# Kernel optimization log

Measured on AMD Instinct MI355X. Metric: run time of the kernel, lower is better.

## Reference

```python
import jax, jax.numpy as jnp
import numpy as np

DIM, HEADS, FEAT = 512, 8, 128
HEAD_DIM = DIM // HEADS
B, N = 1, 2048
EPS = 1e-8


def setup_inputs() -> dict:
    key = jax.random.key(0)
    k1, k2, k3, k4 = jax.random.split(key, 4)
    x = jax.random.normal(k1, (B, N, DIM), dtype=jnp.float32)
    proj_matrix = jax.random.normal(k2, (HEADS, HEAD_DIM, FEAT), dtype=jnp.float32) / np.sqrt(HEAD_DIM)
    W_qkv = jax.random.normal(k3, (DIM, 3 * DIM), dtype=jnp.float32) * np.sqrt(2.0 / DIM)
    W_out = jax.random.normal(k4, (DIM, DIM), dtype=jnp.float32) * np.sqrt(2.0 / DIM)
    b_out = jnp.zeros((DIM,), dtype=jnp.float32)
    return {"x": x, "proj_matrix": proj_matrix, "W_qkv": W_qkv, "W_out": W_out, "b_out": b_out}


def _feature_map(t):
    return jax.nn.elu(t) + 1.0


def reference(x, proj_matrix, W_qkv, W_out, b_out):
    b, n, d = x.shape
    h, hd = HEADS, HEAD_DIM
    qkv = x @ W_qkv                      # (b,n,3d)
    q, k, v = jnp.split(qkv, 3, axis=-1)
    # (b,n,d) -> (b,h,n,hd)
    def to_heads(t):
        return t.reshape(b, n, h, hd).transpose(0, 2, 1, 3)
    q, k, v = to_heads(q), to_heads(k), to_heads(v)
    q_proj = _feature_map(jnp.einsum('bhnd,hdf->bhnf', q, proj_matrix))
    k_proj = _feature_map(jnp.einsum('bhnd,hdf->bhnf', k, proj_matrix))
    # causal linear attention via prefix sums (matches torch cumsum branch)
    k_cum = jnp.cumsum(k_proj, axis=2)                                   # (b,h,n,f)
    kv_cum = jnp.cumsum(k_proj[..., None] * v[..., None, :], axis=2)     # (b,h,n,f,hd)
    attn = jnp.einsum('bhnf,bhnfd->bhnd', q_proj, kv_cum)
    denom = jnp.einsum('bhnf,bhnf->bhn', q_proj, k_cum)[..., None]
    attn = attn / (denom + EPS)
    attn = attn.transpose(0, 2, 1, 3).reshape(b, n, d)
    return attn @ W_out + b_out
```

## Files before the change

kernel.cpp:

```cpp
#include <hip/hip_runtime.h>
#include <math.h>

#define NTOK 2048
#define DMODEL 512
#define NH 8
#define HD 64
#define NF 128
#define QKV_LD 1536
#define CHUNK 64
#define NCHUNK 32
#define EPS_C 1e-8f

typedef __bf16 bf16x8 __attribute__((ext_vector_type(8)));
typedef float f32x4 __attribute__((ext_vector_type(4)));

__device__ inline unsigned short f2bf(float f) {
  union { float f; unsigned u; } v; v.f = f;
  unsigned r = v.u + 0x7FFF + ((v.u >> 16) & 1);
  return (unsigned short)(r >> 16);
}


__global__ __launch_bounds__(256) void pack_all(
    const float* __restrict__ x, const float* __restrict__ W_qkv,
    const float* __restrict__ W_out, const float* __restrict__ proj,
    unsigned short* __restrict__ xpk, unsigned short* __restrict__ wqkvpk,
    unsigned short* __restrict__ woutpk, unsigned short* __restrict__ projpk,
    unsigned short* __restrict__ vT_pk)
{
  const int tid = blockIdx.x * 256 + threadIdx.x;
  const int job = blockIdx.y;
  unsigned short o[8];
  if (job == 0) {
    if (tid >= 131072) return;
    const int lane = tid & 63, blk = tid >> 6;
    const int bk = blk & 15, bm = blk >> 4;
    const int m = bm * 16 + (lane & 15), k = bk * 32 + (lane >> 4) * 8;
    const float4 v0 = *(const float4*)&x[(size_t)m * 512 + k];
    const float4 v1 = *(const float4*)&x[(size_t)m * 512 + k + 4];
    o[0] = f2bf(v0.x); o[1] = f2bf(v0.y); o[2] = f2bf(v0.z); o[3] = f2bf(v0.w);
    o[4] = f2bf(v1.x); o[5] = f2bf(v1.y); o[6] = f2bf(v1.z); o[7] = f2bf(v1.w);
    *(ushort4*)&xpk[(size_t)tid * 8]     = *(ushort4*)&o[0];
    *(ushort4*)&xpk[(size_t)tid * 8 + 4] = *(ushort4*)&o[4];
  } else if (job == 1) {
    if (tid >= 98304) return;
    const int lane = tid & 63, blk = tid >> 6;
    const int bk = blk & 15, bn = blk >> 4;
    const int n = bn * 16 + (lane & 15), k = bk * 32 + (lane >> 4) * 8;
#pragma unroll
    for (int e = 0; e < 8; ++e) o[e] = f2bf(W_qkv[(size_t)(k + e) * QKV_LD + n]);
    *(ushort4*)&wqkvpk[(size_t)tid * 8]     = *(ushort4*)&o[0];
    *(ushort4*)&wqkvpk[(size_t)tid * 8 + 4] = *(ushort4*)&o[4];
  } else if (job == 2) {
    if (tid >= 32768) return;
    const int lane = tid & 63, blk = tid >> 6;
    const int bk = blk & 15, bn = blk >> 4;
    const int n = bn * 16 + (lane & 15), k = bk * 32 + (lane >> 4) * 8;
#pragma unroll
    for (int e = 0; e < 8; ++e) o[e] = f2bf(W_out[(size_t)(k + e) * DMODEL + n]);
    *(ushort4*)&woutpk[(size_t)tid * 8]     = *(ushort4*)&o[0];
    *(ushort4*)&woutpk[(size_t)tid * 8 + 4] = *(ushort4*)&o[4];
  } else if (job == 3) {
    if (tid >= 8192) return;
    const int lane = tid & 63, blk = (tid >> 6) & 15, h = tid >> 10;
    const int bk = blk & 1, bn = blk >> 1;
    const int n = bn * 16 + (lane & 15), k = bk * 32 + (lane >> 4) * 8;
#pragma unroll
    for (int e = 0; e < 8; ++e) o[e] = f2bf(proj[(size_t)h * HD * NF + (size_t)(k + e) * NF + n]);
    *(ushort4*)&projpk[(size_t)tid * 8]     = *(ushort4*)&o[0];
    *(ushort4*)&projpk[(size_t)tid * 8 + 4] = *(ushort4*)&o[4];
  } else {
    if (tid >= 32768) return;
    const int hc = tid >> 7, kt = (tid >> 6) & 1, lane = tid & 63;
    const unsigned short val = ((lane & 15) == 0) ? (unsigned short)0x3F80 : (unsigned short)0;
    const size_t u = (size_t)hc * 640 + (4 * 2 + kt) * 64 + lane;
#pragma unroll
    for (int e = 0; e < 8; ++e) o[e] = val;
    *(ushort4*)&vT_pk[u * 8]     = *(ushort4*)&o[0];
    *(ushort4*)&vT_pk[u * 8 + 4] = *(ushort4*)&o[4];
  }
}

__global__ __launch_bounds__(256) void qkv_proj(
    const unsigned short* __restrict__ Apk, const unsigned short* __restrict__ Bpk,
    const unsigned short* __restrict__ projpk,
    unsigned short* __restrict__ q_pk, unsigned short* __restrict__ k_pk,
    unsigned short* __restrict__ kT_pk, unsigned short* __restrict__ vT_pk)
{
  __shared__ unsigned short QK[4096];
  const int lane = threadIdx.x & 63, w = threadIdx.x >> 6;
  const int wr = w >> 1, wc = w & 1;
  const int c = blockIdx.y;
  const int m0 = c * 64 + wr * 32;
  const int n0 = blockIdx.x * 64 + wc * 32;
  const unsigned short* a0 = Apk + ((size_t)(m0 >> 4) * 16 * 64 + lane) * 8;
  const unsigned short* a1 = a0 + (size_t)16 * 512;
  const unsigned short* b0 = Bpk + ((size_t)(n0 >> 4) * 16 * 64 + lane) * 8;
  const unsigned short* b1 = b0 + (size_t)16 * 512;
  f32x4 acc00 = {0.f, 0.f, 0.f, 0.f}, acc01 = acc00, acc10 = acc00, acc11 = acc00;
#pragma unroll 4
  for (int s = 0; s < 16; ++s) {
    const bf16x8 af0 = *(const bf16x8*)(a0 + (size_t)s * 512);
    const bf16x8 af1 = *(const bf16x8*)(a1 + (size_t)s * 512);
    const bf16x8 bv0 = *(const bf16x8*)(b0 + (size_t)s * 512);
    const bf16x8 bv1 = *(const bf16x8*)(b1 + (size_t)s * 512);
    acc00 = __builtin_amdgcn_mfma_f32_16x16x32_bf16(af0, bv0, acc00, 0, 0, 0);
    acc01 = __builtin_amdgcn_mfma_f32_16x16x32_bf16(af0, bv1, acc01, 0, 0, 0);
    acc10 = __builtin_amdgcn_mfma_f32_16x16x32_bf16(af1, bv0, acc10, 0, 0, 0);
    acc11 = __builtin_amdgcn_mfma_f32_16x16x32_bf16(af1, bv1, acc11, 0, 0, 0);
  }
  const int r16 = lane & 15, kg = lane >> 4;
  if (blockIdx.x < 16) {
    const int src = blockIdx.x >> 3, h = blockIdx.x & 7;
#pragma unroll
    for (int mb = 0; mb < 2; ++mb) {
#pragma unroll
      for (int nb = 0; nb < 2; ++nb) {
        const f32x4 a = mb == 0 ? (nb == 0 ? acc00 : acc01) : (nb == 0 ? acc10 : acc11);
        const size_t u = ((size_t)(wr * 2 + mb) * 2 + wc) * 64 +
                         (nb * 2 + (r16 >> 3)) * 16 + kg * 4;
        const int elem = r16 & 7;
#pragma unroll
        for (int r = 0; r < 4; ++r)
          QK[(u + r) * 8 + elem] = f2bf(a[r]);
      }
    }
    __syncthreads();
    const unsigned short* bbase = projpk + (size_t)h * 8192 + (size_t)lane * 8;
    f32x4 p[2][4] = {};
#pragma unroll
    for (int s = 0; s < 2; ++s) {
#pragma unroll
      for (int mb = 0; mb < 2; ++mb) {
        const bf16x8 af = *(const bf16x8*)&QK[((((size_t)(wr * 2 + mb)) * 2 + s) * 64 + lane) * 8];
#pragma unroll
        for (int nb = 0; nb < 4; ++nb) {
          const bf16x8 bv = *(const bf16x8*)(bbase + (size_t)((wc * 4 + nb) * 2 + s) * 512);
          p[mb][nb] = __builtin_amdgcn_mfma_f32_16x16x32_bf16(af, bv, p[mb][nb], 0, 0, 0);
        }
      }
    }
    unsigned short* dst = (src ? k_pk : q_pk) + (size_t)h * 262144;
#pragma unroll
    for (int mb = 0; mb < 2; ++mb) {
#pragma unroll
      for (int nb = 0; nb < 4; ++nb) {
        unsigned short vb[4];
#pragma unroll
        for (int r = 0; r < 4; ++r) {
          const float v = p[mb][nb][r];
          vb[r] = f2bf(v > 0.f ? v + 1.f : expf(v));
        }
        const size_t base = ((size_t)(c * 4 + wr * 2 + mb) * 4 + wc * 2 + (nb >> 1)) * 64 +
                            ((nb & 1) * 2 + (r16 >> 3)) * 16;
        const int elem = r16 & 7;
#pragma unroll
        for (int r = 0; r < 4; ++r)
          dst[(base + kg * 4 + r) * 8 + elem] = vb[r];
        if (src == 1) {
          const size_t u = (size_t)(h * 32 + c) * 1024 +
              ((size_t)(wc * 4 + nb) * 2 + wr) * 64 + r16 + (mb * 2 + (kg >> 1)) * 16;
          *(ushort4*)&kT_pk[u * 8 + (kg & 1) * 4] = *(ushort4*)&vb[0];
        }
      }
    }
  } else {
    const int h = blockIdx.x - 16;
#pragma unroll
    for (int mb = 0; mb < 2; ++mb) {
#pragma unroll
      for (int nb = 0; nb < 2; ++nb) {
        const f32x4 a = mb == 0 ? (nb == 0 ? acc00 : acc01) : (nb == 0 ? acc10 : acc11);
        const int vc = wc * 32 + nb * 16 + r16;
        const size_t u = (size_t)(h * 32 + c) * 640 +
            ((size_t)(vc >> 4) * 2 + wr) * 64 + (vc & 15) + (mb * 2 + (kg >> 1)) * 16;
        ushort4 rr;
        rr.x = f2bf(a[0]); rr.y = f2bf(a[1]); rr.z = f2bf(a[2]); rr.w = f2bf(a[3]);
        *(ushort4*)&vT_pk[u * 8 + (kg & 1) * 4] = rr;
      }
    }
  }
}

__global__ __launch_bounds__(256) void sums_scan(
    const unsigned short* __restrict__ kT_pk, const unsigned short* __restrict__ vT_pk,
    unsigned short* __restrict__ kvpre_pk)
{
  const int lane = threadIdx.x & 63, w = threadIdx.x >> 6;
  const int vt = blockIdx.x, h = blockIdx.y;
  const int r16 = lane & 15, kg = lane >> 4;
  f32x4 acc[2] = {};
  for (int c = 0; c < NCHUNK; ++c) {
    unsigned short* dst = kvpre_pk + (size_t)(h * 32 + c) * 1280 * 8;
#pragma unroll
    for (int mb = 0; mb < 2; ++mb) {
      unsigned short vb[4];
#pragma unroll
      for (int r = 0; r < 4; ++r) vb[r] = f2bf(acc[mb][r]);
      const size_t u = (size_t)(vt * 4 + w) * 64 + r16 + (mb * 2 + (kg >> 1)) * 16;
      *(ushort4*)&dst[u * 8 + (kg & 1) * 4] = *(ushort4*)&vb[0];
    }
    const unsigned short* kb = kT_pk + (size_t)(h * 32 + c) * 1024 * 8;
    const unsigned short* vb_ = vT_pk + (size_t)(h * 32 + c) * 640 * 8;
#pragma unroll
    for (int s = 0; s < 2; ++s) {
      const bf16x8 bf = *(const bf16x8*)(vb_ + (((size_t)vt * 2 + s) * 64 + lane) * 8);
#pragma unroll
      for (int mb = 0; mb < 2; ++mb) {
        const bf16x8 af = *(const bf16x8*)(kb + ((((size_t)(w * 2 + mb)) * 2 + s) * 64 + lane) * 8);
        acc[mb] = __builtin_amdgcn_mfma_f32_16x16x32_bf16(af, bf, acc[mb], 0, 0, 0);
      }
    }
  }
}

__global__ __launch_bounds__(256) void gemm_out(
    const unsigned short* __restrict__ Apk, const unsigned short* __restrict__ Bpk,
    const float* __restrict__ bias, float* __restrict__ Cf, int K, int ldc)
{
  const int lane = threadIdx.x & 63, w = threadIdx.x >> 6;
  const int wr = w >> 1, wc = w & 1;
  const int m0 = blockIdx.y * 64 + wr * 32;
  const int n0 = blockIdx.x * 64 + wc * 32;
  const int ks = K >> 5;
  const unsigned short* a0 = Apk + ((size_t)(m0 >> 4) * ks * 64 + lane) * 8;
  const unsigned short* a1 = a0 + (size_t)ks * 512;
  const unsigned short* b0 = Bpk + ((size_t)(n0 >> 4) * ks * 64 + lane) * 8;
  const unsigned short* b1 = b0 + (size_t)ks * 512;
  f32x4 acc00 = {0.f, 0.f, 0.f, 0.f}, acc01 = acc00, acc10 = acc00, acc11 = acc00;
#pragma unroll 4
  for (int s = 0; s < ks; ++s) {
    const bf16x8 af0 = *(const bf16x8*)(a0 + (size_t)s * 512);
    const bf16x8 af1 = *(const bf16x8*)(a1 + (size_t)s * 512);
    const bf16x8 bv0 = *(const bf16x8*)(b0 + (size_t)s * 512);
    const bf16x8 bv1 = *(const bf16x8*)(b1 + (size_t)s * 512);
    acc00 = __builtin_amdgcn_mfma_f32_16x16x32_bf16(af0, bv0, acc00, 0, 0, 0);
    acc01 = __builtin_amdgcn_mfma_f32_16x16x32_bf16(af0, bv1, acc01, 0, 0, 0);
    acc10 = __builtin_amdgcn_mfma_f32_16x16x32_bf16(af1, bv0, acc10, 0, 0, 0);
    acc11 = __builtin_amdgcn_mfma_f32_16x16x32_bf16(af1, bv1, acc11, 0, 0, 0);
  }
  const int r16 = lane & 15, kg = lane >> 4;
#pragma unroll
  for (int mb = 0; mb < 2; ++mb) {
#pragma unroll
    for (int nb = 0; nb < 2; ++nb) {
      const f32x4 a = mb == 0 ? (nb == 0 ? acc00 : acc01) : (nb == 0 ? acc10 : acc11);
      const int col = n0 + nb * 16 + r16;
      const float bv = bias[col];
#pragma unroll
      for (int r = 0; r < 4; ++r)
        Cf[(size_t)(m0 + mb * 16 + kg * 4 + r) * ldc + col] = a[r] + bv;
    }
  }
}

__global__ __launch_bounds__(256) void chunk_attn(
    const unsigned short* __restrict__ q_pk, const unsigned short* __restrict__ k_pk,
    const unsigned short* __restrict__ kvpre_pk, const unsigned short* __restrict__ vT_pk,
    unsigned short* __restrict__ attn_pk)
{
  __shared__ unsigned short P[4096];
  __shared__ float den[64];
  const int lane = threadIdx.x & 63, w = threadIdx.x >> 6;
  const int wr = w >> 1, wc = w & 1;
  const int c = blockIdx.x, h = blockIdx.y;
  const int r16 = lane & 15, kg = lane >> 4;
  const unsigned short* qb = q_pk + (size_t)h * 262144;
  const unsigned short* kb = k_pk + (size_t)h * 262144;
  bf16x8 qa[2][4];
#pragma unroll
  for (int amb = 0; amb < 2; ++amb)
#pragma unroll
    for (int ks = 0; ks < 4; ++ks)
      qa[amb][ks] = *(const bf16x8*)(qb +
          (((size_t)(c * 4 + wr * 2 + amb) * 4 + ks) * 64 + lane) * 8);
  {
    f32x4 accS[2][2] = {};
#pragma unroll
    for (int ks = 0; ks < 4; ++ks) {
#pragma unroll
      for (int bnb = 0; bnb < 2; ++bnb) {
        const bf16x8 bf = *(const bf16x8*)(kb +
            (((size_t)(c * 4 + wc * 2 + bnb) * 4 + ks) * 64 + lane) * 8);
#pragma unroll
        for (int amb = 0; amb < 2; ++amb)
          accS[amb][bnb] = __builtin_amdgcn_mfma_f32_16x16x32_bf16(qa[amb][ks], bf, accS[amb][bnb], 0, 0, 0);
      }
    }
#pragma unroll
    for (int amb = 0; amb < 2; ++amb)
#pragma unroll
      for (int bnb = 0; bnb < 2; ++bnb) {
        const int ck = wc * 32 + bnb * 16 + r16;
        const size_t u = ((size_t)(wr * 2 + amb) * 2 + wc) * 64 + (bnb * 2 + (r16 >> 3)) * 16;
        const int elem = r16 & 7;
#pragma unroll
        for (int r = 0; r < 4; ++r) {
          const int rq = wr * 32 + amb * 16 + kg * 4 + r;
          P[(u + kg * 4 + r) * 8 + elem] = (ck <= rq) ? f2bf(accS[amb][bnb][r]) : (unsigned short)0;
        }
      }
  }
  __syncthreads();
  const int nnt = wc ? 2 : 3;
  const int ntb = wc ? 3 : 0;
  const unsigned short* kvp = kvpre_pk + (size_t)(h * 32 + c) * 1280 * 8;
  const unsigned short* vtb = vT_pk + (size_t)(h * 32 + c) * 640 * 8;
  f32x4 acc[2][3] = {};
#pragma unroll
  for (int ks = 0; ks < 4; ++ks) {
    bf16x8 bfr[3];
    for (int j = 0; j < 3; ++j)
      if (j < nnt)
        bfr[j] = *(const bf16x8*)(kvp + (((size_t)(ntb + j) * 4 + ks) * 64 + lane) * 8);
#pragma unroll
    for (int amb = 0; amb < 2; ++amb)
      for (int j = 0; j < 3; ++j)
        if (j < nnt)
          acc[amb][j] = __builtin_amdgcn_mfma_f32_16x16x32_bf16(qa[amb][ks], bfr[j], acc[amb][j], 0, 0, 0);
  }
#pragma unroll
  for (int ks = 0; ks < 2; ++ks) {
    bf16x8 bfr[3];
    for (int j = 0; j < 3; ++j)
      if (j < nnt)
        bfr[j] = *(const bf16x8*)(vtb + (((size_t)(ntb + j) * 2 + ks) * 64 + lane) * 8);
#pragma unroll
    for (int amb = 0; amb < 2; ++amb) {
      const bf16x8 pf = *(const bf16x8*)&P[((((size_t)(wr * 2 + amb)) * 2 + ks) * 64 + lane) * 8];
      for (int j = 0; j < 3; ++j)
        if (j < nnt)
          acc[amb][j] = __builtin_amdgcn_mfma_f32_16x16x32_bf16(pf, bfr[j], acc[amb][j], 0, 0, 0);
    }
  }
  if (wc == 1 && r16 == 0) {
#pragma unroll
    for (int amb = 0; amb < 2; ++amb)
#pragma unroll
      for (int r = 0; r < 4; ++r)
        den[wr * 32 + amb * 16 + kg * 4 + r] = acc[amb][1][r] + EPS_C;
  }
  __syncthreads();
#pragma unroll
  for (int amb = 0; amb < 2; ++amb) {
    for (int j = 0; j < 3; ++j) {
      const int nt = ntb + j;
      if (nt >= 4 || j >= nnt) continue;
      const int acol = h * 64 + nt * 16 + r16;
      const size_t base = ((size_t)(c * 4 + wr * 2 + amb) * 16 + (acol >> 5)) * 64 +
                          ((nt * 2 + (r16 >> 3)) & 3) * 16;
      const int elem = acol & 7;
#pragma unroll
      for (int r = 0; r < 4; ++r) {
        const float dinv = 1.0f / den[wr * 32 + amb * 16 + kg * 4 + r];
        attn_pk[(base + kg * 4 + r) * 8 + elem] = f2bf(acc[amb][j][r] * dinv);
      }
    }
  }
}

extern "C" void kernel_launch(void* const* d_in, const int* in_sizes, int n_in,
                              void* d_out, int out_size, void* d_ws, size_t ws_size,
                              hipStream_t stream) {
  const float* x     = (const float*)d_in[0];
  const float* proj  = (const float*)d_in[1];
  const float* W_qkv = (const float*)d_in[2];
  const float* W_out = (const float*)d_in[3];
  const float* b_out = (const float*)d_in[4];
  float* out = (float*)d_out;

  unsigned short* xpk      = (unsigned short*)d_ws;
  unsigned short* wqkvpk   = xpk + 1048576;
  unsigned short* woutpk   = wqkvpk + 786432;
  unsigned short* projpk   = woutpk + 262144;
  unsigned short* q_pk     = projpk + 65536;
  unsigned short* k_pk     = q_pk + 2097152;
  unsigned short* kT_pk    = k_pk + 2097152;
  unsigned short* vT_pk    = kT_pk + 2097152;
  unsigned short* kvpre_pk = vT_pk + 1310720;
  unsigned short* attn_pk  = kvpre_pk + 2621440;

  pack_all<<<dim3(512, 5), 256, 0, stream>>>(x, W_qkv, W_out, proj,
                                             xpk, wqkvpk, woutpk, projpk, vT_pk);
  qkv_proj<<<dim3(QKV_LD / 64, NTOK / 64), 256, 0, stream>>>(
      xpk, wqkvpk, projpk, q_pk, k_pk, kT_pk, vT_pk);
  sums_scan<<<dim3(5, NH), 256, 0, stream>>>(kT_pk, vT_pk, kvpre_pk);
  chunk_attn<<<dim3(NCHUNK, NH), 256, 0, stream>>>(
      q_pk, k_pk, kvpre_pk, vT_pk, attn_pk);
  gemm_out<<<dim3(DMODEL / 64, NTOK / 64), 256, 0, stream>>>(
      attn_pk, woutpk, b_out, out, DMODEL, DMODEL);
}
```

Measured before the change: 52.56 us.

## Fuse all five stages into one cooperative persistent kernel with grid syncs

Turns the five separate kernels into device functions with grid-stride loops and runs them inside one cooperative kernel, separated by grid-wide barriers. The grid is sized from occupancy queries (256 CUs times up to 3 blocks each). If the cooperative launch fails, it falls back to separate launches. The goal is to remove the launch gaps between stages, at the cost of grid-sync overhead, a persistent grid that may be too large for tiny phases like the 40-block scan, and an occupancy query on every call.

```diff
diff --git a/kernel.cpp b/kernel.cpp
--- a/kernel.cpp
+++ b/kernel.cpp
@@ -1,5 +1,8 @@
 #include <hip/hip_runtime.h>
+#include <hip/hip_cooperative_groups.h>
 #include <math.h>
+
+namespace cg = cooperative_groups;
 
 #define NTOK 2048
 #define DMODEL 512
@@ -21,343 +24,398 @@
 }
 
 
-__global__ __launch_bounds__(256) void pack_all(
-    const float* __restrict__ x, const float* __restrict__ W_qkv,
-    const float* __restrict__ W_out, const float* __restrict__ proj,
-    unsigned short* __restrict__ xpk, unsigned short* __restrict__ wqkvpk,
-    unsigned short* __restrict__ woutpk, unsigned short* __restrict__ projpk,
-    unsigned short* __restrict__ vT_pk)
-{
-  const int tid = blockIdx.x * 256 + threadIdx.x;
-  const int job = blockIdx.y;
-  unsigned short o[8];
-  if (job == 0) {
-    if (tid >= 131072) return;
-    const int lane = tid & 63, blk = tid >> 6;
-    const int bk = blk & 15, bm = blk >> 4;
-    const int m = bm * 16 + (lane & 15), k = bk * 32 + (lane >> 4) * 8;
-    const float4 v0 = *(const float4*)&x[(size_t)m * 512 + k];
-    const float4 v1 = *(const float4*)&x[(size_t)m * 512 + k + 4];
-    o[0] = f2bf(v0.x); o[1] = f2bf(v0.y); o[2] = f2bf(v0.z); o[3] = f2bf(v0.w);
-    o[4] = f2bf(v1.x); o[5] = f2bf(v1.y); o[6] = f2bf(v1.z); o[7] = f2bf(v1.w);
-    *(ushort4*)&xpk[(size_t)tid * 8]     = *(ushort4*)&o[0];
-    *(ushort4*)&xpk[(size_t)tid * 8 + 4] = *(ushort4*)&o[4];
-  } else if (job == 1) {
-    if (tid >= 98304) return;
-    const int lane = tid & 63, blk = tid >> 6;
-    const int bk = blk & 15, bn = blk >> 4;
-    const int n = bn * 16 + (lane & 15), k = bk * 32 + (lane >> 4) * 8;
-#pragma unroll
-    for (int e = 0; e < 8; ++e) o[e] = f2bf(W_qkv[(size_t)(k + e) * QKV_LD + n]);
-    *(ushort4*)&wqkvpk[(size_t)tid * 8]     = *(ushort4*)&o[0];
-    *(ushort4*)&wqkvpk[(size_t)tid * 8 + 4] = *(ushort4*)&o[4];
-  } else if (job == 2) {
-    if (tid >= 32768) return;
-    const int lane = tid & 63, blk = tid >> 6;
-    const int bk = blk & 15, bn = blk >> 4;
-    const int n = bn * 16 + (lane & 15), k = bk * 32 + (lane >> 4) * 8;
-#pragma unroll
-    for (int e = 0; e < 8; ++e) o[e] = f2bf(W_out[(size_t)(k + e) * DMODEL + n]);
-    *(ushort4*)&woutpk[(size_t)tid * 8]     = *(ushort4*)&o[0];
-    *(ushort4*)&woutpk[(size_t)tid * 8 + 4] = *(ushort4*)&o[4];
-  } else if (job == 3) {
-    if (tid >= 8192) return;
-    const int lane = tid & 63, blk = (tid >> 6) & 15, h = tid >> 10;
-    const int bk = blk & 1, bn = blk >> 1;
-    const int n = bn * 16 + (lane & 15), k = bk * 32 + (lane >> 4) * 8;
-#pragma unroll
-    for (int e = 0; e < 8; ++e) o[e] = f2bf(proj[(size_t)h * HD * NF + (size_t)(k + e) * NF + n]);
-    *(ushort4*)&projpk[(size_t)tid * 8]     = *(ushort4*)&o[0];
-    *(ushort4*)&projpk[(size_t)tid * 8 + 4] = *(ushort4*)&o[4];
-  } else {
-    if (tid >= 32768) return;
-    const int hc = tid >> 7, kt = (tid >> 6) & 1, lane = tid & 63;
-    const unsigned short val = ((lane & 15) == 0) ? (unsigned short)0x3F80 : (unsigned short)0;
-    const size_t u = (size_t)hc * 640 + (4 * 2 + kt) * 64 + lane;
-#pragma unroll
-    for (int e = 0; e < 8; ++e) o[e] = val;
-    *(ushort4*)&vT_pk[u * 8]     = *(ushort4*)&o[0];
-    *(ushort4*)&vT_pk[u * 8 + 4] = *(ushort4*)&o[4];
-  }
-}
-
-__global__ __launch_bounds__(256) void qkv_proj(
-    const unsigned short* __restrict__ Apk, const unsigned short* __restrict__ Bpk,
-    const unsigned short* __restrict__ projpk,
-    unsigned short* __restrict__ q_pk, unsigned short* __restrict__ k_pk,
-    unsigned short* __restrict__ kT_pk, unsigned short* __restrict__ vT_pk)
+__device__ void ph_pack(
+    const float* x, const float* W_qkv, const float* W_out, const float* proj,
+    unsigned short* xpk, unsigned short* wqkvpk, unsigned short* woutpk,
+    unsigned short* projpk, unsigned short* vT_pk)
+{
+  for (int v = blockIdx.x; v < 1184; v += gridDim.x) {
+    unsigned short o[8];
+    if (v < 512) {
+      const int tid = v * 256 + threadIdx.x;
+      const int lane = tid & 63, blk = tid >> 6;
+      const int bk = blk & 15, bm = blk >> 4;
+      const int m = bm * 16 + (lane & 15), k = bk * 32 + (lane >> 4) * 8;
+      const float4 v0 = *(const float4*)&x[(size_t)m * 512 + k];
+      const float4 v1 = *(const float4*)&x[(size_t)m * 512 + k + 4];
+      o[0] = f2bf(v0.x); o[1] = f2bf(v0.y); o[2] = f2bf(v0.z); o[3] = f2bf(v0.w);
+      o[4] = f2bf(v1.x); o[5] = f2bf(v1.y); o[6] = f2bf(v1.z); o[7] = f2bf(v1.w);
+      *(ushort4*)&xpk[(size_t)tid * 8]     = *(ushort4*)&o[0];
+      *(ushort4*)&xpk[(size_t)tid * 8 + 4] = *(ushort4*)&o[4];
+    } else if (v < 896) {
+      const int tid = (v - 512) * 256 + threadIdx.x;
+      const int lane = tid & 63, blk = tid >> 6;
+      const int bk = blk & 15, bn = blk >> 4;
+      const int n = bn * 16 + (lane & 15), k = bk * 32 + (lane >> 4) * 8;
+#pragma unroll
+      for (int e = 0; e < 8; ++e) o[e] = f2bf(W_qkv[(size_t)(k + e) * QKV_LD + n]);
+      *(ushort4*)&wqkvpk[(size_t)tid * 8]     = *(ushort4*)&o[0];
+      *(ushort4*)&wqkvpk[(size_t)tid * 8 + 4] = *(ushort4*)&o[4];
+    } else if (v < 1024) {
+      const int tid = (v - 896) * 256 + threadIdx.x;
+      const int lane = tid & 63, blk = tid >> 6;
+      const int bk = blk & 15, bn = blk >> 4;
+      const int n = bn * 16 + (lane & 15), k = bk * 32 + (lane >> 4) * 8;
+#pragma unroll
+      for (int e = 0; e < 8; ++e) o[e] = f2bf(W_out[(size_t)(k + e) * DMODEL + n]);
+      *(ushort4*)&woutpk[(size_t)tid * 8]     = *(ushort4*)&o[0];
+      *(ushort4*)&woutpk[(size_t)tid * 8 + 4] = *(ushort4*)&o[4];
+    } else if (v < 1056) {
+      const int tid = (v - 1024) * 256 + threadIdx.x;
+      const int lane = tid & 63, blk = (tid >> 6) & 15, h = tid >> 10;
+      const int bk = blk & 1, bn = blk >> 1;
+      const int n = bn * 16 + (lane & 15), k = bk * 32 + (lane >> 4) * 8;
+#pragma unroll
+      for (int e = 0; e < 8; ++e) o[e] = f2bf(proj[(size_t)h * HD * NF + (size_t)(k + e) * NF + n]);
+      *(ushort4*)&projpk[(size_t)tid * 8]     = *(ushort4*)&o[0];
+      *(ushort4*)&projpk[(size_t)tid * 8 + 4] = *(ushort4*)&o[4];
+    } else {
+      const int tid = (v - 1056) * 256 + threadIdx.x;
+      const int hc = tid >> 7, kt = (tid >> 6) & 1, lane = tid & 63;
+      const unsigned short val = ((lane & 15) == 0) ? (unsigned short)0x3F80 : (unsigned short)0;
+      const size_t u = (size_t)hc * 640 + (4 * 2 + kt) * 64 + lane;
+#pragma unroll
+      for (int e = 0; e < 8; ++e) o[e] = val;
+      *(ushort4*)&vT_pk[u * 8]     = *(ushort4*)&o[0];
+      *(ushort4*)&vT_pk[u * 8 + 4] = *(ushort4*)&o[4];
+    }
+  }
+}
+
+__device__ void ph_qkvproj(
+    const unsigned short* Apk, const unsigned short* Bpk,
+    const unsigned short* projpk, unsigned short* q_pk, unsigned short* k_pk,
+    unsigned short* kT_pk, unsigned short* vT_pk)
 {
   __shared__ unsigned short QK[4096];
   const int lane = threadIdx.x & 63, w = threadIdx.x >> 6;
   const int wr = w >> 1, wc = w & 1;
-  const int c = blockIdx.y;
-  const int m0 = c * 64 + wr * 32;
-  const int n0 = blockIdx.x * 64 + wc * 32;
-  const unsigned short* a0 = Apk + ((size_t)(m0 >> 4) * 16 * 64 + lane) * 8;
-  const unsigned short* a1 = a0 + (size_t)16 * 512;
-  const unsigned short* b0 = Bpk + ((size_t)(n0 >> 4) * 16 * 64 + lane) * 8;
-  const unsigned short* b1 = b0 + (size_t)16 * 512;
-  f32x4 acc00 = {0.f, 0.f, 0.f, 0.f}, acc01 = acc00, acc10 = acc00, acc11 = acc00;
+  const int r16 = lane & 15, kg = lane >> 4;
+  for (int j = blockIdx.x; j < 768; j += gridDim.x) {
+    const int bx = j % 24, c = j / 24;
+    const int m0 = c * 64 + wr * 32;
+    const int n0 = bx * 64 + wc * 32;
+    const unsigned short* a0 = Apk + ((size_t)(m0 >> 4) * 16 * 64 + lane) * 8;
+    const unsigned short* a1 = a0 + (size_t)16 * 512;
+    const unsigned short* b0 = Bpk + ((size_t)(n0 >> 4) * 16 * 64 + lane) * 8;
+    const unsigned short* b1 = b0 + (size_t)16 * 512;
+    f32x4 acc00 = {0.f, 0.f, 0.f, 0.f}, acc01 = acc00, acc10 = acc00, acc11 = acc00;
 #pragma unroll 4
-  for (int s = 0; s < 16; ++s) {
-    const bf16x8 af0 = *(const bf16x8*)(a0 + (size_t)s * 512);
-    const bf16x8 af1 = *(const bf16x8*)(a1 + (size_t)s * 512);
-    const bf16x8 bv0 = *(const bf16x8*)(b0 + (size_t)s * 512);
-    const bf16x8 bv1 = *(const bf16x8*)(b1 + (size_t)s * 512);
-    acc00 = __builtin_amdgcn_mfma_f32_16x16x32_bf16(af0, bv0, acc00, 0, 0, 0);
-    acc01 = __builtin_amdgcn_mfma_f32_16x16x32_bf16(af0, bv1, acc01, 0, 0, 0);
-    acc10 = __builtin_amdgcn_mfma_f32_16x16x32_bf16(af1, bv0, acc10, 0, 0, 0);
-    acc11 = __builtin_amdgcn_mfma_f32_16x16x32_bf16(af1, bv1, acc11, 0, 0, 0);
-  }
+    for (int s = 0; s < 16; ++s) {
+      const bf16x8 af0 = *(const bf16x8*)(a0 + (size_t)s * 512);
+      const bf16x8 af1 = *(const bf16x8*)(a1 + (size_t)s * 512);
+      const bf16x8 bv0 = *(const bf16x8*)(b0 + (size_t)s * 512);
+      const bf16x8 bv1 = *(const bf16x8*)(b1 + (size_t)s * 512);
+      acc00 = __builtin_amdgcn_mfma_f32_16x16x32_bf16(af0, bv0, acc00, 0, 0, 0);
+      acc01 = __builtin_amdgcn_mfma_f32_16x16x32_bf16(af0, bv1, acc01, 0, 0, 0);
+      acc10 = __builtin_amdgcn_mfma_f32_16x16x32_bf16(af1, bv0, acc10, 0, 0, 0);
+      acc11 = __builtin_amdgcn_mfma_f32_16x16x32_bf16(af1, bv1, acc11, 0, 0, 0);
+    }
+    if (bx < 16) {
+      const int src = bx >> 3, h = bx & 7;
+#pragma unroll
+      for (int mb = 0; mb < 2; ++mb) {
+#pragma unroll
+        for (int nb = 0; nb < 2; ++nb) {
+          const f32x4 a = mb == 0 ? (nb == 0 ? acc00 : acc01) : (nb == 0 ? acc10 : acc11);
+          const size_t u = ((size_t)(wr * 2 + mb) * 2 + wc) * 64 +
+                           (nb * 2 + (r16 >> 3)) * 16 + kg * 4;
+          const int elem = r16 & 7;
+#pragma unroll
+          for (int r = 0; r < 4; ++r)
+            QK[(u + r) * 8 + elem] = f2bf(a[r]);
+        }
+      }
+      __syncthreads();
+      const unsigned short* bbase = projpk + (size_t)h * 8192 + (size_t)lane * 8;
+      f32x4 p[2][4] = {};
+#pragma unroll
+      for (int s = 0; s < 2; ++s) {
+#pragma unroll
+        for (int mb = 0; mb < 2; ++mb) {
+          const bf16x8 af = *(const bf16x8*)&QK[((((size_t)(wr * 2 + mb)) * 2 + s) * 64 + lane) * 8];
+#pragma unroll
+          for (int nb = 0; nb < 4; ++nb) {
+            const bf16x8 bv = *(const bf16x8*)(bbase + (size_t)((wc * 4 + nb) * 2 + s) * 512);
+            p[mb][nb] = __builtin_amdgcn_mfma_f32_16x16x32_bf16(af, bv, p[mb][nb], 0, 0, 0);
+          }
+        }
+      }
+      unsigned short* dst = (src ? k_pk : q_pk) + (size_t)h * 262144;
+#pragma unroll
+      for (int mb = 0; mb < 2; ++mb) {
+#pragma unroll
+        for (int nb = 0; nb < 4; ++nb) {
+          unsigned short vb[4];
+#pragma unroll
+          for (int r = 0; r < 4; ++r) {
+            const float vv = p[mb][nb][r];
+            vb[r] = f2bf(vv > 0.f ? vv + 1.f : expf(vv));
+          }
+          const size_t base = ((size_t)(c * 4 + wr * 2 + mb) * 4 + wc * 2 + (nb >> 1)) * 64 +
+                              ((nb & 1) * 2 + (r16 >> 3)) * 16;
+          const int elem = r16 & 7;
+#pragma unroll
+          for (int r = 0; r < 4; ++r)
+            dst[(base + kg * 4 + r) * 8 + elem] = vb[r];
+          if (src == 1) {
+            const size_t u = (size_t)(h * 32 + c) * 1024 +
+                ((size_t)(wc * 4 + nb) * 2 + wr) * 64 + r16 + (mb * 2 + (kg >> 1)) * 16;
+            *(ushort4*)&kT_pk[u * 8 + (kg & 1) * 4] = *(ushort4*)&vb[0];
+          }
+        }
+      }
+      __syncthreads();
+    } else {
+      const int h = bx - 16;
+#pragma unroll
+      for (int mb = 0; mb < 2; ++mb) {
+#pragma unroll
+        for (int nb = 0; nb < 2; ++nb) {
+          const f32x4 a = mb == 0 ? (nb == 0 ? acc00 : acc01) : (nb == 0 ? acc10 : acc11);
+          const int vc = wc * 32 + nb * 16 + r16;
+          const size_t u = (size_t)(h * 32 + c) * 640 +
+              ((size_t)(vc >> 4) * 2 + wr) * 64 + (vc & 15) + (mb * 2 + (kg >> 1)) * 16;
+          ushort4 rr;
+          rr.x = f2bf(a[0]); rr.y = f2bf(a[1]); rr.z = f2bf(a[2]); rr.w = f2bf(a[3]);
+          *(ushort4*)&vT_pk[u * 8 + (kg & 1) * 4] = rr;
+        }
+      }
+    }
+  }
+}
+
+__device__ void ph_scan(
+    const unsigned short* kT_pk, const unsigned short* vT_pk,
+    unsigned short* kvpre_pk)
+{
+  const int lane = threadIdx.x & 63, w = threadIdx.x >> 6;
   const int r16 = lane & 15, kg = lane >> 4;
-  if (blockIdx.x < 16) {
-    const int src = blockIdx.x >> 3, h = blockIdx.x & 7;
-#pragma unroll
-    for (int mb = 0; mb < 2; ++mb) {
-#pragma unroll
-      for (int nb = 0; nb < 2; ++nb) {
-        const f32x4 a = mb == 0 ? (nb == 0 ? acc00 : acc01) : (nb == 0 ? acc10 : acc11);
-        const size_t u = ((size_t)(wr * 2 + mb) * 2 + wc) * 64 +
-                         (nb * 2 + (r16 >> 3)) * 16 + kg * 4;
-        const int elem = r16 & 7;
-#pragma unroll
-        for (int r = 0; r < 4; ++r)
-          QK[(u + r) * 8 + elem] = f2bf(a[r]);
-      }
-    }
-    __syncthreads();
-    const unsigned short* bbase = projpk + (size_t)h * 8192 + (size_t)lane * 8;
-    f32x4 p[2][4] = {};
-#pragma unroll
-    for (int s = 0; s < 2; ++s) {
+  for (int j = blockIdx.x; j < 40; j += gridDim.x) {
+    const int vt = j % 5, h = j / 5;
+    f32x4 acc[2] = {};
+    for (int c = 0; c < NCHUNK; ++c) {
+      unsigned short* dst = kvpre_pk + (size_t)(h * 32 + c) * 1280 * 8;
 #pragma unroll
       for (int mb = 0; mb < 2; ++mb) {
-        const bf16x8 af = *(const bf16x8*)&QK[((((size_t)(wr * 2 + mb)) * 2 + s) * 64 + lane) * 8];
-#pragma unroll
-        for (int nb = 0; nb < 4; ++nb) {
-          const bf16x8 bv = *(const bf16x8*)(bbase + (size_t)((wc * 4 + nb) * 2 + s) * 512);
-          p[mb][nb] = __builtin_amdgcn_mfma_f32_16x16x32_bf16(af, bv, p[mb][nb], 0, 0, 0);
-        }
-      }
-    }
-    unsigned short* dst = (src ? k_pk : q_pk) + (size_t)h * 262144;
-#pragma unroll
-    for (int mb = 0; mb < 2; ++mb) {
-#pragma unroll
-      for (int nb = 0; nb < 4; ++nb) {
         unsigned short vb[4];
 #pragma unroll
-        for (int r = 0; r < 4; ++r) {
-          const float v = p[mb][nb][r];
-          vb[r] = f2bf(v > 0.f ? v + 1.f : expf(v));
-        }
-        const size_t base = ((size_t)(c * 4 + wr * 2 + mb) * 4 + wc * 2 + (nb >> 1)) * 64 +
-                            ((nb & 1) * 2 + (r16 >> 3)) * 16;
-        const int elem = r16 & 7;
-#pragma unroll
-        for (int r = 0; r < 4; ++r)
-          dst[(base + kg * 4 + r) * 8 + elem] = vb[r];
-        if (src == 1) {
-          const size_t u = (size_t)(h * 32 + c) * 1024 +
-              ((size_t)(wc * 4 + nb) * 2 + wr) * 64 + r16 + (mb * 2 + (kg >> 1)) * 16;
-          *(ushort4*)&kT_pk[u * 8 + (kg & 1) * 4] = *(ushort4*)&vb[0];
-        }
-      }
-    }
-  } else {
-    const int h = blockIdx.x - 16;
-#pragma unroll
-    for (int mb = 0; mb < 2; ++mb) {
-#pragma unroll
-      for (int nb = 0; nb < 2; ++nb) {
-        const f32x4 a = mb == 0 ? (nb == 0 ? acc00 : acc01) : (nb == 0 ? acc10 : acc11);
-        const int vc = wc * 32 + nb * 16 + r16;
-        const size_t u = (size_t)(h * 32 + c) * 640 +
-            ((size_t)(vc >> 4) * 2 + wr) * 64 + (vc & 15) + (mb * 2 + (kg >> 1)) * 16;
-        ushort4 rr;
-        rr.x = f2bf(a[0]); rr.y = f2bf(a[1]); rr.z = f2bf(a[2]); rr.w = f2bf(a[3]);
-        *(ushort4*)&vT_pk[u * 8 + (kg & 1) * 4] = rr;
-      }
-    }
-  }
-}
-
-__global__ __launch_bounds__(256) void sums_scan(
-    const unsigned short* __restrict__ kT_pk, const unsigned short* __restrict__ vT_pk,
-    unsigned short* __restrict__ kvpre_pk)
-{
-  const int lane = threadIdx.x & 63, w = threadIdx.x >> 6;
-  const int vt = blockIdx.x, h = blockIdx.y;
-  const int r16 = lane & 15, kg = lane >> 4;
-  f32x4 acc[2] = {};
-  for (int c = 0; c < NCHUNK; ++c) {
-    unsigned short* dst = kvpre_pk + (size_t)(h * 32 + c) * 1280 * 8;
-#pragma unroll
-    for (int mb = 0; mb < 2; ++mb) {
-      unsigned short vb[4];
-#pragma unroll
-      for (int r = 0; r < 4; ++r) vb[r] = f2bf(acc[mb][r]);
-      const size_t u = (size_t)(vt * 4 + w) * 64 + r16 + (mb * 2 + (kg >> 1)) * 16;
-      *(ushort4*)&dst[u * 8 + (kg & 1) * 4] = *(ushort4*)&vb[0];
-    }
-    const unsigned short* kb = kT_pk + (size_t)(h * 32 + c) * 1024 * 8;
-    const unsigned short* vb_ = vT_pk + (size_t)(h * 32 + c) * 640 * 8;
-#pragma unroll
-    for (int s = 0; s < 2; ++s) {
-      const bf16x8 bf = *(const bf16x8*)(vb_ + (((size_t)vt * 2 + s) * 64 + lane) * 8);
-#pragma unroll
-      for (int mb = 0; mb < 2; ++mb) {
-        const bf16x8 af = *(const bf16x8*)(kb + ((((size_t)(w * 2 + mb)) * 2 + s) * 64 + lane) * 8);
-        acc[mb] = __builtin_amdgcn_mfma_f32_16x16x32_bf16(af, bf, acc[mb], 0, 0, 0);
-      }
-    }
-  }
-}
-
-__global__ __launch_bounds__(256) void gemm_out(
-    const unsigned short* __restrict__ Apk, const unsigned short* __restrict__ Bpk,
-    const float* __restrict__ bias, float* __restrict__ Cf, int K, int ldc)
-{
-  const int lane = threadIdx.x & 63, w = threadIdx.x >> 6;
-  const int wr = w >> 1, wc = w & 1;
-  const int m0 = blockIdx.y * 64 + wr * 32;
-  const int n0 = blockIdx.x * 64 + wc * 32;
-  const int ks = K >> 5;
-  const unsigned short* a0 = Apk + ((size_t)(m0 >> 4) * ks * 64 + lane) * 8;
-  const unsigned short* a1 = a0 + (size_t)ks * 512;
-  const unsigned short* b0 = Bpk + ((size_t)(n0 >> 4) * ks * 64 + lane) * 8;
-  const unsigned short* b1 = b0 + (size_t)ks * 512;
-  f32x4 acc00 = {0.f, 0.f, 0.f, 0.f}, acc01 = acc00, acc10 = acc00, acc11 = acc00;
-#pragma unroll 4
-  for (int s = 0; s < ks; ++s) {
-    const bf16x8 af0 = *(const bf16x8*)(a0 + (size_t)s * 512);
-    const bf16x8 af1 = *(const bf16x8*)(a1 + (size_t)s * 512);
-    const bf16x8 bv0 = *(const bf16x8*)(b0 + (size_t)s * 512);
-    const bf16x8 bv1 = *(const bf16x8*)(b1 + (size_t)s * 512);
-    acc00 = __builtin_amdgcn_mfma_f32_16x16x32_bf16(af0, bv0, acc00, 0, 0, 0);
-    acc01 = __builtin_amdgcn_mfma_f32_16x16x32_bf16(af0, bv1, acc01, 0, 0, 0);
-    acc10 = __builtin_amdgcn_mfma_f32_16x16x32_bf16(af1, bv0, acc10, 0, 0, 0);
-    acc11 = __builtin_amdgcn_mfma_f32_16x16x32_bf16(af1, bv1, acc11, 0, 0, 0);
-  }
-  const int r16 = lane & 15, kg = lane >> 4;
-#pragma unroll
-  for (int mb = 0; mb < 2; ++mb) {
-#pragma unroll
-    for (int nb = 0; nb < 2; ++nb) {
-      const f32x4 a = mb == 0 ? (nb == 0 ? acc00 : acc01) : (nb == 0 ? acc10 : acc11);
-      const int col = n0 + nb * 16 + r16;
-      const float bv = bias[col];
-#pragma unroll
-      for (int r = 0; r < 4; ++r)
-        Cf[(size_t)(m0 + mb * 16 + kg * 4 + r) * ldc + col] = a[r] + bv;
-    }
-  }
-}
-
-__global__ __launch_bounds__(256) void chunk_attn(
-    const unsigned short* __restrict__ q_pk, const unsigned short* __restrict__ k_pk,
-    const unsigned short* __restrict__ kvpre_pk, const unsigned short* __restrict__ vT_pk,
-    unsigned short* __restrict__ attn_pk)
+        for (int r = 0; r < 4; ++r) vb[r] = f2bf(acc[mb][r]);
+        const size_t u = (size_t)(vt * 4 + w) * 64 + r16 + (mb * 2 + (kg >> 1)) * 16;
+        *(ushort4*)&dst[u * 8 + (kg & 1) * 4] = *(ushort4*)&vb[0];
+      }
+      const unsigned short* kb = kT_pk + (size_t)(h * 32 + c) * 1024 * 8;
+      const unsigned short* vb_ = vT_pk + (size_t)(h * 32 + c) * 640 * 8;
+#pragma unroll
+      for (int s = 0; s < 2; ++s) {
+        const bf16x8 bf = *(const bf16x8*)(vb_ + (((size_t)vt * 2 + s) * 64 + lane) * 8);
+#pragma unroll
+        for (int mb = 0; mb < 2; ++mb) {
+          const bf16x8 af = *(const bf16x8*)(kb + ((((size_t)(w * 2 + mb)) * 2 + s) * 64 + lane) * 8);
+          acc[mb] = __builtin_amdgcn_mfma_f32_16x16x32_bf16(af, bf, acc[mb], 0, 0, 0);
+        }
+      }
+    }
+  }
+}
+
+__device__ void ph_attn(
+    const unsigned short* q_pk, const unsigned short* k_pk,
+    const unsigned short* kvpre_pk, const unsigned short* vT_pk,
+    unsigned short* attn_pk)
 {
   __shared__ unsigned short P[4096];
   __shared__ float den[64];
   const int lane = threadIdx.x & 63, w = threadIdx.x >> 6;
   const int wr = w >> 1, wc = w & 1;
-  const int c = blockIdx.x, h = blockIdx.y;
   const int r16 = lane & 15, kg = lane >> 4;
-  const unsigned short* qb = q_pk + (size_t)h * 262144;
-  const unsigned short* kb = k_pk + (size_t)h * 262144;
-  bf16x8 qa[2][4];
-#pragma unroll
-  for (int amb = 0; amb < 2; ++amb)
-#pragma unroll
-    for (int ks = 0; ks < 4; ++ks)
-      qa[amb][ks] = *(const bf16x8*)(qb +
-          (((size_t)(c * 4 + wr * 2 + amb) * 4 + ks) * 64 + lane) * 8);
-  {
-    f32x4 accS[2][2] = {};
+  for (int j = blockIdx.x; j < 256; j += gridDim.x) {
+    const int c = j % 32, h = j / 32;
+    const unsigned short* qb = q_pk + (size_t)h * 262144;
+    const unsigned short* kb = k_pk + (size_t)h * 262144;
+    bf16x8 qa[2][4];
+#pragma unroll
+    for (int amb = 0; amb < 2; ++amb)
+#pragma unroll
+      for (int ks = 0; ks < 4; ++ks)
+        qa[amb][ks] = *(const bf16x8*)(qb +
+            (((size_t)(c * 4 + wr * 2 + amb) * 4 + ks) * 64 + lane) * 8);
+    {
+      f32x4 accS[2][2] = {};
+#pragma unroll
+      for (int ks = 0; ks < 4; ++ks) {
+#pragma unroll
+        for (int bnb = 0; bnb < 2; ++bnb) {
+          const bf16x8 bf = *(const bf16x8*)(kb +
+              (((size_t)(c * 4 + wc * 2 + bnb) * 4 + ks) * 64 + lane) * 8);
+#pragma unroll
+          for (int amb = 0; amb < 2; ++amb)
+            accS[amb][bnb] = __builtin_amdgcn_mfma_f32_16x16x32_bf16(qa[amb][ks], bf, accS[amb][bnb], 0, 0, 0);
+        }
+      }
+#pragma unroll
+      for (int amb = 0; amb < 2; ++amb)
+#pragma unroll
+        for (int bnb = 0; bnb < 2; ++bnb) {
+          const int ck = wc * 32 + bnb * 16 + r16;
+          const size_t u = ((size_t)(wr * 2 + amb) * 2 + wc) * 64 + (bnb * 2 + (r16 >> 3)) * 16;
+          const int elem = r16 & 7;
+#pragma unroll
+          for (int r = 0; r < 4; ++r) {
+            const int rq = wr * 32 + amb * 16 + kg * 4 + r;
+            P[(u + kg * 4 + r) * 8 + elem] = (ck <= rq) ? f2bf(accS[amb][bnb][r]) : (unsigned short)0;
+          }
+        }
+    }
+    __syncthreads();
+    const int nnt = wc ? 2 : 3;
+    const int ntb = wc ? 3 : 0;
+    const unsigned short* kvp = kvpre_pk + (size_t)(h * 32 + c) * 1280 * 8;
+    const unsigned short* vtb = vT_pk + (size_t)(h * 32 + c) * 640 * 8;
+    f32x4 acc[2][3] = {};
 #pragma unroll
     for (int ks = 0; ks < 4; ++ks) {
-#pragma unroll
-      for (int bnb = 0; bnb < 2; ++bnb) {
-        const bf16x8 bf = *(const bf16x8*)(kb +
-            (((size_t)(c * 4 + wc * 2 + bnb) * 4 + ks) * 64 + lane) * 8);
-#pragma unroll
-        for (int amb = 0; amb < 2; ++amb)
-          accS[amb][bnb] = __builtin_amdgcn_mfma_f32_16x16x32_bf16(qa[amb][ks], bf, accS[amb][bnb], 0, 0, 0);
-      }
-    }
-#pragma unroll
-    for (int amb = 0; amb < 2; ++amb)
-#pragma unroll
-      for (int bnb = 0; bnb < 2; ++bnb) {
-        const int ck = wc * 32 + bnb * 16 + r16;
-        const size_t u = ((size_t)(wr * 2 + amb) * 2 + wc) * 64 + (bnb * 2 + (r16 >> 3)) * 16;
-        const int elem = r16 & 7;
+      bf16x8 bfr[3];
+      for (int jj = 0; jj < 3; ++jj)
+        if (jj < nnt)
+          bfr[jj] = *(const bf16x8*)(kvp + (((size_t)(ntb + jj) * 4 + ks) * 64 + lane) * 8);
+#pragma unroll
+      for (int amb = 0; amb < 2; ++amb)
+        for (int jj = 0; jj < 3; ++jj)
+          if (jj < nnt)
+            acc[amb][jj] = __builtin_amdgcn_mfma_f32_16x16x32_bf16(qa[amb][ks], bfr[jj], acc[amb][jj], 0, 0, 0);
+    }
+#pragma unroll
+    for (int ks = 0; ks < 2; ++ks) {
+      bf16x8 bfr[3];
+      for (int jj = 0; jj < 3; ++jj)
+        if (jj < nnt)
+          bfr[jj] = *(const bf16x8*)(vtb + (((size_t)(ntb + jj) * 2 + ks) * 64 + lane) * 8);
+#pragma unroll
+      for (int amb = 0; amb < 2; ++amb) {
+        const bf16x8 pf = *(const bf16x8*)&P[((((size_t)(wr * 2 + amb)) * 2 + ks) * 64 + lane) * 8];
+        for (int jj = 0; jj < 3; ++jj)
+          if (jj < nnt)
+            acc[amb][jj] = __builtin_amdgcn_mfma_f32_16x16x32_bf16(pf, bfr[jj], acc[amb][jj], 0, 0, 0);
+      }
+    }
+    if (wc == 1 && r16 == 0) {
+#pragma unroll
+      for (int amb = 0; amb < 2; ++amb)
+#pragma unroll
+        for (int r = 0; r < 4; ++r)
+          den[wr * 32 + amb * 16 + kg * 4 + r] = acc[amb][1][r] + EPS_C;
+    }
+    __syncthreads();
+#pragma unroll
+    for (int amb = 0; amb < 2; ++amb) {
+      for (int jj = 0; jj < 3; ++jj) {
+        const int nt = ntb + jj;
+        if (nt >= 4 || jj >= nnt) continue;
+        const int acol = h * 64 + nt * 16 + r16;
+        const size_t base = ((size_t)(c * 4 + wr * 2 + amb) * 16 + (acol >> 5)) * 64 +
+                            ((nt * 2 + (r16 >> 3)) & 3) * 16;
+        const int elem = acol & 7;
 #pragma unroll
         for (int r = 0; r < 4; ++r) {
-          const int rq = wr * 32 + amb * 16 + kg * 4 + r;
-          P[(u + kg * 4 + r) * 8 + elem] = (ck <= rq) ? f2bf(accS[amb][bnb][r]) : (unsigned short)0;
-        }
-      }
-  }
-  __syncthreads();
-  const int nnt = wc ? 2 : 3;
-  const int ntb = wc ? 3 : 0;
-  const unsigned short* kvp = kvpre_pk + (size_t)(h * 32 + c) * 1280 * 8;
-  const unsigned short* vtb = vT_pk + (size_t)(h * 32 + c) * 640 * 8;
-  f32x4 acc[2][3] = {};
-#pragma unroll
-  for (int ks = 0; ks < 4; ++ks) {
-    bf16x8 bfr[3];
-    for (int j = 0; j < 3; ++j)
-      if (j < nnt)
-        bfr[j] = *(const bf16x8*)(kvp + (((size_t)(ntb + j) * 4 + ks) * 64 + lane) * 8);
-#pragma unroll
-    for (int amb = 0; amb < 2; ++amb)
-      for (int j = 0; j < 3; ++j)
-        if (j < nnt)
-          acc[amb][j] = __builtin_amdgcn_mfma_f32_16x16x32_bf16(qa[amb][ks], bfr[j], acc[amb][j], 0, 0, 0);
-  }
-#pragma unroll
-  for (int ks = 0; ks < 2; ++ks) {
-    bf16x8 bfr[3];
-    for (int j = 0; j < 3; ++j)
-      if (j < nnt)
-        bfr[j] = *(const bf16x8*)(vtb + (((size_t)(ntb + j) * 2 + ks) * 64 + lane) * 8);
-#pragma unroll
-    for (int amb = 0; amb < 2; ++amb) {
-      const bf16x8 pf = *(const bf16x8*)&P[((((size_t)(wr * 2 + amb)) * 2 + ks) * 64 + lane) * 8];
-      for (int j = 0; j < 3; ++j)
-        if (j < nnt)
-          acc[amb][j] = __builtin_amdgcn_mfma_f32_16x16x32_bf16(pf, bfr[j], acc[amb][j], 0, 0, 0);
-    }
-  }
-  if (wc == 1 && r16 == 0) {
-#pragma unroll
-    for (int amb = 0; amb < 2; ++amb)
-#pragma unroll
-      for (int r = 0; r < 4; ++r)
-        den[wr * 32 + amb * 16 + kg * 4 + r] = acc[amb][1][r] + EPS_C;
-  }
-  __syncthreads();
-#pragma unroll
-  for (int amb = 0; amb < 2; ++amb) {
-    for (int j = 0; j < 3; ++j) {
-      const int nt = ntb + j;
-      if (nt >= 4 || j >= nnt) continue;
-      const int acol = h * 64 + nt * 16 + r16;
-      const size_t base = ((size_t)(c * 4 + wr * 2 + amb) * 16 + (acol >> 5)) * 64 +
-                          ((nt * 2 + (r16 >> 3)) & 3) * 16;
-      const int elem = acol & 7;
-#pragma unroll
-      for (int r = 0; r < 4; ++r) {
-        const float dinv = 1.0f / den[wr * 32 + amb * 16 + kg * 4 + r];
-        attn_pk[(base + kg * 4 + r) * 8 + elem] = f2bf(acc[amb][j][r] * dinv);
-      }
-    }
-  }
-}
+          const float dinv = 1.0f / den[wr * 32 + amb * 16 + kg * 4 + r];
+          attn_pk[(base + kg * 4 + r) * 8 + elem] = f2bf(acc[amb][jj][r] * dinv);
+        }
+      }
+    }
+    __syncthreads();
+  }
+}
+
+__device__ void ph_out(
+    const unsigned short* Apk, const unsigned short* Bpk,
+    const float* bias, float* Cf)
+{
+  const int lane = threadIdx.x & 63, w = threadIdx.x >> 6;
+  const int wr = w >> 1, wc = w & 1;
+  const int r16 = lane & 15, kg = lane >> 4;
+  for (int j = blockIdx.x; j < 256; j += gridDim.x) {
+    const int nx = j % 8, my = j / 8;
+    const int m0 = my * 64 + wr * 32;
+    const int n0 = nx * 64 + wc * 32;
+    const unsigned short* a0 = Apk + ((size_t)(m0 >> 4) * 16 * 64 + lane) * 8;
+    const unsigned short* a1 = a0 + (size_t)16 * 512;
+    const unsigned short* b0 = Bpk + ((size_t)(n0 >> 4) * 16 * 64 + lane) * 8;
+    const unsigned short* b1 = b0 + (size_t)16 * 512;
+    f32x4 acc00 = {0.f, 0.f, 0.f, 0.f}, acc01 = acc00, acc10 = acc00, acc11 = acc00;
+#pragma unroll 4
+    for (int s = 0; s < 16; ++s) {
+      const bf16x8 af0 = *(const bf16x8*)(a0 + (size_t)s * 512);
+      const bf16x8 af1 = *(const bf16x8*)(a1 + (size_t)s * 512);
+      const bf16x8 bv0 = *(const bf16x8*)(b0 + (size_t)s * 512);
+      const bf16x8 bv1 = *(const bf16x8*)(b1 + (size_t)s * 512);
+      acc00 = __builtin_amdgcn_mfma_f32_16x16x32_bf16(af0, bv0, acc00, 0, 0, 0);
+      acc01 = __builtin_amdgcn_mfma_f32_16x16x32_bf16(af0, bv1, acc01, 0, 0, 0);
+      acc10 = __builtin_amdgcn_mfma_f32_16x16x32_bf16(af1, bv0, acc10, 0, 0, 0);
+      acc11 = __builtin_amdgcn_mfma_f32_16x16x32_bf16(af1, bv1, acc11, 0, 0, 0);
+    }
+#pragma unroll
+    for (int mb = 0; mb < 2; ++mb) {
+#pragma unroll
+      for (int nb = 0; nb < 2; ++nb) {
+        const f32x4 a = mb == 0 ? (nb == 0 ? acc00 : acc01) : (nb == 0 ? acc10 : acc11);
+        const int col = n0 + nb * 16 + r16;
+        const float bv = bias[col];
+#pragma unroll
+        for (int r = 0; r < 4; ++r)
+          Cf[(size_t)(m0 + mb * 16 + kg * 4 + r) * 512 + col] = a[r] + bv;
+      }
+    }
+  }
+}
+
+__global__ __launch_bounds__(256) void mega(
+    const float* x, const float* proj, const float* W_qkv, const float* W_out,
+    const float* b_out, float* out,
+    unsigned short* xpk, unsigned short* wqkvpk, unsigned short* woutpk,
+    unsigned short* projpk, unsigned short* q_pk, unsigned short* k_pk,
+    unsigned short* kT_pk, unsigned short* vT_pk, unsigned short* kvpre_pk,
+    unsigned short* attn_pk)
+{
+  cg::grid_group g = cg::this_grid();
+  ph_pack(x, W_qkv, W_out, proj, xpk, wqkvpk, woutpk, projpk, vT_pk);
+  g.sync();
+  ph_qkvproj(xpk, wqkvpk, projpk, q_pk, k_pk, kT_pk, vT_pk);
+  g.sync();
+  ph_scan(kT_pk, vT_pk, kvpre_pk);
+  g.sync();
+  ph_attn(q_pk, k_pk, kvpre_pk, vT_pk, attn_pk);
+  g.sync();
+  ph_out(attn_pk, woutpk, b_out, out);
+}
+
+__global__ __launch_bounds__(256) void k_pack(
+    const float* x, const float* W_qkv, const float* W_out, const float* proj,
+    unsigned short* xpk, unsigned short* wqkvpk, unsigned short* woutpk,
+    unsigned short* projpk, unsigned short* vT_pk)
+{ ph_pack(x, W_qkv, W_out, proj, xpk, wqkvpk, woutpk, projpk, vT_pk); }
+
+__global__ __launch_bounds__(256) void k_qkvproj(
+    const unsigned short* Apk, const unsigned short* Bpk,
+    const unsigned short* projpk, unsigned short* q_pk, unsigned short* k_pk,
+    unsigned short* kT_pk, unsigned short* vT_pk)
+{ ph_qkvproj(Apk, Bpk, projpk, q_pk, k_pk, kT_pk, vT_pk); }
+
+__global__ __launch_bounds__(256) void k_scan(
+    const unsigned short* kT_pk, const unsigned short* vT_pk,
+    unsigned short* kvpre_pk)
+{ ph_scan(kT_pk, vT_pk, kvpre_pk); }
+
+__global__ __launch_bounds__(256) void k_attn(
+    const unsigned short* q_pk, const unsigned short* k_pk,
+    const unsigned short* kvpre_pk, const unsigned short* vT_pk,
+    unsigned short* attn_pk)
+{ ph_attn(q_pk, k_pk, kvpre_pk, vT_pk, attn_pk); }
+
+__global__ __launch_bounds__(256) void k_out(
+    const unsigned short* Apk, const unsigned short* Bpk,
+    const float* bias, float* Cf)
+{ ph_out(Apk, Bpk, bias, Cf); }
 
 extern "C" void kernel_launch(void* const* d_in, const int* in_sizes, int n_in,
                               void* d_out, int out_size, void* d_ws, size_t ws_size,
@@ -380,13 +438,25 @@
   unsigned short* kvpre_pk = vT_pk + 1310720;
   unsigned short* attn_pk  = kvpre_pk + 2621440;
 
-  pack_all<<<dim3(512, 5), 256, 0, stream>>>(x, W_qkv, W_out, proj,
-                                             xpk, wqkvpk, woutpk, projpk, vT_pk);
-  qkv_proj<<<dim3(QKV_LD / 64, NTOK / 64), 256, 0, stream>>>(
-      xpk, wqkvpk, projpk, q_pk, k_pk, kT_pk, vT_pk);
-  sums_scan<<<dim3(5, NH), 256, 0, stream>>>(kT_pk, vT_pk, kvpre_pk);
-  chunk_attn<<<dim3(NCHUNK, NH), 256, 0, stream>>>(
-      q_pk, k_pk, kvpre_pk, vT_pk, attn_pk);
-  gemm_out<<<dim3(DMODEL / 64, NTOK / 64), 256, 0, stream>>>(
-      attn_pk, woutpk, b_out, out, DMODEL, DMODEL);
-}
+  int occ = 0;
+  (void)hipOccupancyMaxActiveBlocksPerMultiprocessor(&occ, (const void*)mega, 256, 0);
+  if (occ < 1) occ = 1;
+  if (occ > 3) occ = 3;
+  const int nblk = 256 * occ;
+
+  void* args[] = {
+    (void*)&x, (void*)&proj, (void*)&W_qkv, (void*)&W_out, (void*)&b_out,
+    (void*)&out, (void*)&xpk, (void*)&wqkvpk, (void*)&woutpk, (void*)&projpk,
+    (void*)&q_pk, (void*)&k_pk, (void*)&kT_pk, (void*)&vT_pk, (void*)&kvpre_pk,
+    (void*)&attn_pk };
+  const hipError_t le = hipLaunchCooperativeKernel(
+      (const void*)mega, dim3(nblk), dim3(256), args, 0, stream);
+  if (le != hipSuccess) {
+    k_pack<<<1184, 256, 0, stream>>>(x, W_qkv, W_out, proj,
+                                     xpk, wqkvpk, woutpk, projpk, vT_pk);
+    k_qkvproj<<<768, 256, 0, stream>>>(xpk, wqkvpk, projpk, q_pk, k_pk, kT_pk, vT_pk);
+    k_scan<<<40, 256, 0, stream>>>(kT_pk, vT_pk, kvpre_pk);
+    k_attn<<<256, 256, 0, stream>>>(q_pk, k_pk, kvpre_pk, vT_pk, attn_pk);
+    k_out<<<256, 256, 0, stream>>>(attn_pk, woutpk, b_out, out);
+  }
+}
```

Result: slower. 194.9 us (+270.8%).
